# Performance work log

Hardware: AMD Instinct MI355X
Metric: run time of the kernel (lower is better)

## Reference

```python
import jax, jax.numpy as jnp
import numpy as np

B, D_IN, C, P = 8192, 2048, 1000, 256


def setup_inputs() -> dict:
    key = jax.random.key(0)
    ks = jax.random.split(key, 6)
    return {
        "x": jax.random.normal(ks[0], (B, D_IN), dtype=jnp.float32),
        "Wm": jax.random.normal(ks[1], (C, D_IN), dtype=jnp.float32) * (1.0 / np.sqrt(D_IN)),
        "bm": jax.random.normal(ks[2], (C,), dtype=jnp.float32) * 0.01,
        "u": jax.random.normal(ks[3], (P, C), dtype=jnp.float32),
        "v": jax.random.normal(ks[4], (P, C), dtype=jnp.float32),
        "w": jax.random.normal(ks[5], (P, 1), dtype=jnp.float32),
    }


def reference(x, Wm, bm, u, v, w):
    # Backbone: Linear(D_IN -> C) producing per-instance logits (B, C)
    preds = jnp.einsum("bd,cd->bc", x, Wm) + bm
    # Gated attention, fully batched (replaces per-instance Python loop):
    # tanh(u @ pred) * sigmoid(v @ pred)  -> (B, P)
    gated = jnp.tanh(jnp.einsum("bc,pc->bp", preds, u)) * jax.nn.sigmoid(
        jnp.einsum("bc,pc->bp", preds, v)
    )
    scores = (gated @ w).ravel()          # (B,)
    attention = jax.nn.softmax(scores)    # softmax over instances
    total_pred = jnp.sum(preds * attention[:, None])
    return preds, total_pred
```

## Files before the change

### kernel.cpp

```cpp
#include <hip/hip_runtime.h>
#include <hip/hip_fp16.h>

typedef _Float16 half8 __attribute__((ext_vector_type(8)));
typedef float f32x4 __attribute__((ext_vector_type(4)));

#define B_   8192
#define DIN  2048
#define C_   1000
#define CP   1024
#define NP2  512

static const size_t OFF_WH  = 0;
static const size_t OFF_UVH = OFF_WH  + (size_t)CP * DIN * 2;
static const size_t OFF_PH  = OFF_UVH + (size_t)NP2 * CP * 2;
static const size_t OFF_SC  = OFF_PH  + (size_t)B_ * CP * 2;
static const size_t OFF_RS  = OFF_SC  + (size_t)B_ * 4;
static const size_t WS_NEED = OFF_RS  + (size_t)B_ * 4;

__device__ __forceinline__ void gload16(const void* g, void* l) {
  __builtin_amdgcn_global_load_lds(
      (const __attribute__((address_space(1))) void*)g,
      (__attribute__((address_space(3))) void*)l, 16, 0, 0);
}

__global__ __launch_bounds__(256) void prep_kernel(
    const float* __restrict__ Wm,
    const float* __restrict__ u, const float* __restrict__ v,
    _Float16* __restrict__ wh, _Float16* __restrict__ uvh,
    float* __restrict__ scores, float* __restrict__ rowsum)
{
  const long NW  = (long)CP * DIN / 8;
  const long NUV = (long)NP2 * CP / 8;
  const long NZ  = 2 * (long)B_ / 8;
  const long T   = NW + NUV + NZ;
  for (long idx = (long)blockIdx.x * blockDim.x + threadIdx.x; idx < T;
       idx += (long)gridDim.x * blockDim.x) {
    if (idx < NW) {
      long e = idx * 8;
      int row = (int)(e >> 11);
      half8 h;
      if (row < C_) {
        float4 p0 = *(const float4*)(Wm + e);
        float4 p1 = *(const float4*)(Wm + e + 4);
        h[0] = (_Float16)p0.x; h[1] = (_Float16)p0.y; h[2] = (_Float16)p0.z; h[3] = (_Float16)p0.w;
        h[4] = (_Float16)p1.x; h[5] = (_Float16)p1.y; h[6] = (_Float16)p1.z; h[7] = (_Float16)p1.w;
      } else {
        h = (half8)(_Float16)0.f;
      }
      *(half8*)(wh + e) = h;
    } else if (idx < NW + NUV) {
      long e = (idx - NW) * 8;
      int j = (int)(e >> 10);
      int k = (int)(e & 1023);
      const float* src = (j & 1) ? v : u;
      int p = j >> 1;
      half8 h;
      #pragma unroll
      for (int t = 0; t < 8; ++t) {
        int kk = k + t;
        h[t] = (kk < C_) ? (_Float16)src[(size_t)p * C_ + kk] : (_Float16)0.f;
      }
      *(half8*)(uvh + e) = h;
    } else {
      long e = (idx - NW - NUV) * 8;
      float4 z = {0.f, 0.f, 0.f, 0.f};
      if (e < B_) {
        *(float4*)(scores + e) = z; *(float4*)(scores + e + 4) = z;
      } else {
        long r = e - B_;
        *(float4*)(rowsum + r) = z; *(float4*)(rowsum + r + 4) = z;
      }
    }
  }
}

__global__ __launch_bounds__(256) void gemm1_kernel(
    const float* __restrict__ x, const _Float16* __restrict__ wh,
    const float* __restrict__ bmv, float* __restrict__ preds,
    _Float16* __restrict__ predsh, float* __restrict__ rowsum)
{
  __shared__ _Float16 sA[2][128 * 64];
  __shared__ _Float16 sB[2][128 * 64];
  const int tid  = threadIdx.x;
  const int lane = tid & 63;
  const int w    = tid >> 6;
  const int wm   = w >> 1, wn = w & 1;
  const int bm0  = blockIdx.x * 128;
  const int bn0  = blockIdx.y * 128;

  f32x4 acc[4][4] = {};

  const float* srcA[4];
  int dstAoff[4];
  #pragma unroll
  for (int i = 0; i < 4; ++i) {
    int slot = i * 256 + tid;
    int row  = slot >> 3;
    int cb   = (slot & 7) << 4;
    dstAoff[i] = row * 128 + (cb ^ ((row & 7) << 4));
    srcA[i] = x + (size_t)(bm0 + row) * DIN + (slot & 7) * 8;
  }
  const _Float16* srcB[4];
  #pragma unroll
  for (int i = 0; i < 4; ++i) {
    int slot = i * 256 + tid;
    int row  = slot >> 3;
    int cb   = (slot & 7) << 4;
    int scb  = cb ^ ((row & 7) << 4);
    srcB[i] = wh + (size_t)(bn0 + row) * DIN + (scb >> 1);
  }
  int aoff[4][2], boff[4][2];
  #pragma unroll
  for (int mi = 0; mi < 4; ++mi) {
    #pragma unroll
    for (int ks = 0; ks < 2; ++ks) {
      int kb = ks * 64 + (lane >> 4) * 16;
      int ra = wm * 64 + mi * 16 + (lane & 15);
      aoff[mi][ks] = ra * 128 + (kb ^ ((ra & 7) << 4));
      int rb = wn * 64 + mi * 16 + (lane & 15);
      boff[mi][ks] = rb * 128 + (kb ^ ((rb & 7) << 4));
    }
  }

  float4 ra[4][2];
  auto loadA = [&]() {
    #pragma unroll
    for (int i = 0; i < 4; ++i) {
      ra[i][0] = *(const float4*)(srcA[i]);
      ra[i][1] = *(const float4*)(srcA[i] + 4);
      srcA[i] += 64;
    }
  };
  auto writeA = [&](int c) {
    #pragma unroll
    for (int i = 0; i < 4; ++i) {
      half8 h;
      h[0] = (_Float16)ra[i][0].x; h[1] = (_Float16)ra[i][0].y;
      h[2] = (_Float16)ra[i][0].z; h[3] = (_Float16)ra[i][0].w;
      h[4] = (_Float16)ra[i][1].x; h[5] = (_Float16)ra[i][1].y;
      h[6] = (_Float16)ra[i][1].z; h[7] = (_Float16)ra[i][1].w;
      *(half8*)((char*)&sA[c][0] + dstAoff[i]) = h;
    }
  };
  auto stageB = [&](int c) {
    #pragma unroll
    for (int i = 0; i < 4; ++i) {
      gload16(srcB[i], &sB[c][(i * 4 + w) * 512]);
      srcB[i] += 64;
    }
  };
  auto compute = [&](int c) {
    const char* bA = (const char*)&sA[c][0];
    const char* bB = (const char*)&sB[c][0];
    #pragma unroll
    for (int ks = 0; ks < 2; ++ks) {
      half8 a[4], b[4];
      #pragma unroll
      for (int mi = 0; mi < 4; ++mi) a[mi] = *(const half8*)(bA + aoff[mi][ks]);
      #pragma unroll
      for (int ni = 0; ni < 4; ++ni) b[ni] = *(const half8*)(bB + boff[ni][ks]);
      #pragma unroll
      for (int mi = 0; mi < 4; ++mi)
        #pragma unroll
        for (int ni = 0; ni < 4; ++ni)
          acc[mi][ni] = __builtin_amdgcn_mfma_f32_16x16x32_f16(a[mi], b[ni], acc[mi][ni], 0, 0, 0);
    }
  };

  const int NT = DIN / 64;

  loadA();
  stageB(0);
  writeA(0);
  asm volatile("s_waitcnt vmcnt(0) lgkmcnt(0)" ::: "memory");
  __builtin_amdgcn_s_barrier();

  #pragma unroll 1
  for (int t = 0; t < NT - 1; ++t) {
    const int c = t & 1;
    loadA();
    stageB(c ^ 1);
    asm volatile("s_waitcnt vmcnt(12)" ::: "memory");
    __builtin_amdgcn_s_barrier();
    compute(c);
    writeA(c ^ 1);
    asm volatile("s_waitcnt lgkmcnt(0)" ::: "memory");
    __builtin_amdgcn_s_barrier();
  }
  asm volatile("s_waitcnt vmcnt(0)" ::: "memory");
  __builtin_amdgcn_s_barrier();
  compute((NT - 1) & 1);

  float rp[4][4] = {};
  #pragma unroll
  for (int mi = 0; mi < 4; ++mi) {
    #pragma unroll
    for (int ni = 0; ni < 4; ++ni) {
      f32x4 d = acc[mi][ni];
      int gc = bn0 + wn * 64 + ni * 16 + (lane & 15);
      float bias = (gc < C_) ? bmv[gc] : 0.f;
      #pragma unroll
      for (int j = 0; j < 4; ++j) {
        int gr = bm0 + wm * 64 + mi * 16 + (lane >> 4) * 4 + j;
        float val = d[j] + bias;
        predsh[(size_t)gr * CP + gc] = (_Float16)val;
        if (gc < C_) preds[(size_t)gr * C_ + gc] = val;
        rp[mi][j] += val;
      }
    }
  }
  #pragma unroll
  for (int mi = 0; mi < 4; ++mi) {
    #pragma unroll
    for (int j = 0; j < 4; ++j) {
      float s = rp[mi][j];
      s += __shfl_xor(s, 1); s += __shfl_xor(s, 2);
      s += __shfl_xor(s, 4); s += __shfl_xor(s, 8);
      if ((lane & 15) == 0) {
        int gr = bm0 + wm * 64 + mi * 16 + (lane >> 4) * 4 + j;
        atomicAdd(&rowsum[gr], s);
      }
    }
  }
}

__global__ __launch_bounds__(256) void gemm2_kernel(
    const _Float16* __restrict__ predsh, const _Float16* __restrict__ uvh,
    const float* __restrict__ wv, float* __restrict__ scores)
{
  __shared__ _Float16 sA[2][64 * 64];
  __shared__ _Float16 sB[2][128 * 64];
  const int tid  = threadIdx.x;
  const int lane = tid & 63;
  const int w    = tid >> 6;
  const int wm   = w >> 1, wn = w & 1;
  const int bm0  = blockIdx.x * 64;
  const int bn0  = blockIdx.y * 128;

  f32x4 acc[2][4] = {};

  const _Float16* srcA[2]; const _Float16* srcB[4];
  #pragma unroll
  for (int i = 0; i < 2; ++i) {
    int slot = i * 256 + tid;
    int row  = slot >> 3;
    int cb   = (slot & 7) << 4;
    int scb  = cb ^ ((row & 7) << 4);
    srcA[i] = predsh + (size_t)(bm0 + row) * CP + (scb >> 1);
  }
  #pragma unroll
  for (int i = 0; i < 4; ++i) {
    int slot = i * 256 + tid;
    int row  = slot >> 3;
    int cb   = (slot & 7) << 4;
    int scb  = cb ^ ((row & 7) << 4);
    srcB[i] = uvh + (size_t)(bn0 + row) * CP + (scb >> 1);
  }
  int aoff[2][2], boff[4][2];
  #pragma unroll
  for (int ks = 0; ks < 2; ++ks) {
    int kb = ks * 64 + (lane >> 4) * 16;
    #pragma unroll
    for (int mi = 0; mi < 2; ++mi) {
      int ra = wm * 32 + mi * 16 + (lane & 15);
      aoff[mi][ks] = ra * 128 + (kb ^ ((ra & 7) << 4));
    }
    #pragma unroll
    for (int ni = 0; ni < 4; ++ni) {
      int rb = wn * 64 + ni * 16 + (lane & 15);
      boff[ni][ks] = rb * 128 + (kb ^ ((rb & 7) << 4));
    }
  }

  auto stage = [&](int c) {
    #pragma unroll
    for (int i = 0; i < 2; ++i) {
      gload16(srcA[i], &sA[c][(i * 4 + w) * 512]);
      srcA[i] += 64;
    }
    #pragma unroll
    for (int i = 0; i < 4; ++i) {
      gload16(srcB[i], &sB[c][(i * 4 + w) * 512]);
      srcB[i] += 64;
    }
  };

  auto compute = [&](int c) {
    const char* bA = (const char*)&sA[c][0];
    const char* bB = (const char*)&sB[c][0];
    #pragma unroll
    for (int ks = 0; ks < 2; ++ks) {
      half8 a[2], b[4];
      #pragma unroll
      for (int mi = 0; mi < 2; ++mi) a[mi] = *(const half8*)(bA + aoff[mi][ks]);
      #pragma unroll
      for (int ni = 0; ni < 4; ++ni) b[ni] = *(const half8*)(bB + boff[ni][ks]);
      #pragma unroll
      for (int mi = 0; mi < 2; ++mi)
        #pragma unroll
        for (int ni = 0; ni < 4; ++ni)
          acc[mi][ni] = __builtin_amdgcn_mfma_f32_16x16x32_f16(a[mi], b[ni], acc[mi][ni], 0, 0, 0);
    }
  };

  const int NT = CP / 64;
  stage(0);
  #pragma unroll 1
  for (int kt = 0; kt < NT; kt += 2) {
    stage(1);
    asm volatile("s_waitcnt vmcnt(6)" ::: "memory");
    __builtin_amdgcn_s_barrier();
    compute(0);
    __builtin_amdgcn_s_barrier();
    if (kt + 2 < NT) {
      stage(0);
      asm volatile("s_waitcnt vmcnt(6)" ::: "memory");
    } else {
      asm volatile("s_waitcnt vmcnt(0)" ::: "memory");
    }
    __builtin_amdgcn_s_barrier();
    compute(1);
    __builtin_amdgcn_s_barrier();
  }

  float sp[2][4] = {};
  #pragma unroll
  for (int mi = 0; mi < 2; ++mi) {
    #pragma unroll
    for (int ni = 0; ni < 4; ++ni) {
      f32x4 d = acc[mi][ni];
      int gc = bn0 + wn * 64 + ni * 16 + (lane & 15);
      float wq = wv[gc >> 1];
      bool even = ((gc & 1) == 0);
      #pragma unroll
      for (int j = 0; j < 4; ++j) {
        float t  = d[j];
        float pr = __shfl_xor(t, 1);
        float th = 2.f / (1.f + __expf(-2.f * t)) - 1.f;
        float sg = 1.f / (1.f + __expf(-pr));
        sp[mi][j] += even ? (th * sg * wq) : 0.f;
      }
    }
  }
  #pragma unroll
  for (int mi = 0; mi < 2; ++mi) {
    #pragma unroll
    for (int j = 0; j < 4; ++j) {
      float s = sp[mi][j];
      s += __shfl_xor(s, 1); s += __shfl_xor(s, 2);
      s += __shfl_xor(s, 4); s += __shfl_xor(s, 8);
      if ((lane & 15) == 0) {
        int gr = bm0 + wm * 32 + mi * 16 + (lane >> 4) * 4 + j;
        atomicAdd(&scores[gr], s);
      }
    }
  }
}

__global__ __launch_bounds__(1024) void final_kernel(
    const float* __restrict__ scores, const float* __restrict__ rowsum,
    float* __restrict__ out)
{
  __shared__ float red[16], red2[16];
  const int t = threadIdx.x;
  const int lane = t & 63, wid = t >> 6;
  float s[8];
  float m = -3.4e38f;
  #pragma unroll
  for (int i = 0; i < 8; ++i) { s[i] = scores[t + i * 1024]; m = fmaxf(m, s[i]); }
  #pragma unroll
  for (int off = 1; off < 64; off <<= 1) m = fmaxf(m, __shfl_xor(m, off));
  if (lane == 0) red[wid] = m;
  __syncthreads();
  #pragma unroll
  for (int i = 0; i < 16; ++i) m = fmaxf(m, red[i]);
  __syncthreads();

  float se = 0.f, sr = 0.f;
  #pragma unroll
  for (int i = 0; i < 8; ++i) {
    float e = __expf(s[i] - m);
    se += e;
    sr += e * rowsum[t + i * 1024];
  }
  #pragma unroll
  for (int off = 1; off < 64; off <<= 1) { se += __shfl_xor(se, off); sr += __shfl_xor(sr, off); }
  if (lane == 0) { red[wid] = se; red2[wid] = sr; }
  __syncthreads();
  if (t == 0) {
    float tse = 0.f, tsr = 0.f;
    for (int i = 0; i < 16; ++i) { tse += red[i]; tsr += red2[i]; }
    out[0] = tsr / tse;
  }
}

extern "C" void kernel_launch(void* const* d_in, const int* in_sizes, int n_in,
                              void* d_out, int out_size, void* d_ws, size_t ws_size,
                              hipStream_t stream)
{
  const float* x   = (const float*)d_in[0];
  const float* Wm  = (const float*)d_in[1];
  const float* bmv = (const float*)d_in[2];
  const float* u   = (const float*)d_in[3];
  const float* v   = (const float*)d_in[4];
  const float* wv  = (const float*)d_in[5];
  float* out = (float*)d_out;

  if (ws_size < WS_NEED) return;

  char* ws = (char*)d_ws;
  _Float16* wh     = (_Float16*)(ws + OFF_WH);
  _Float16* uvh    = (_Float16*)(ws + OFF_UVH);
  _Float16* predsh = (_Float16*)(ws + OFF_PH);
  float*    scores = (float*)(ws + OFF_SC);
  float*    rowsum = (float*)(ws + OFF_RS);

  prep_kernel<<<1288, 256, 0, stream>>>(Wm, u, v, wh, uvh, scores, rowsum);
  gemm1_kernel<<<dim3(64, 8), 256, 0, stream>>>(x, wh, bmv, out, predsh, rowsum);
  gemm2_kernel<<<dim3(128, 4), 256, 0, stream>>>(predsh, uvh, wv, scores);
  final_kernel<<<1, 1024, 0, stream>>>(scores, rowsum, out + (size_t)B_ * C_);
}
```

Measured before the change: 92.93 us.

## Restructure gemm1 into 512-thread triple-buffered pipeline with fp32 LDS staging

Rewrites the first GEMM so that fp32 x tiles are loaded straight into LDS with global_load_lds, and the fp16 conversion happens after LDS reads rather than through registers. Each block now has 512 threads covering 256 rows, k-steps are 32, and a three-deep buffer ring lets fragment reads for the next step overlap MFMAs on the current one. MFMA sections are wrapped in raised wave priority. The goal is to hide global load latency and drop the register round-trip for A, at the cost of more LDS (about 120KB) and twice as many LDS bytes read for A.

```diff
diff --git a/kernel.cpp b/kernel.cpp
--- a/kernel.cpp
+++ b/kernel.cpp
@@ -16,6 +16,12 @@
 static const size_t OFF_SC  = OFF_PH  + (size_t)B_ * CP * 2;
 static const size_t OFF_RS  = OFF_SC  + (size_t)B_ * 4;
 static const size_t WS_NEED = OFF_RS  + (size_t)B_ * 4;
+
+#define FENCE asm volatile("" ::: "memory")
+#define BARRIER do { FENCE; __builtin_amdgcn_s_barrier(); FENCE; } while (0)
+#define VMCNT(n) asm volatile("s_waitcnt vmcnt(" #n ")" ::: "memory")
+#define PRIO1 __builtin_amdgcn_s_setprio(1)
+#define PRIO0 __builtin_amdgcn_s_setprio(0)
 
 __device__ __forceinline__ void gload16(const void* g, void* l) {
   __builtin_amdgcn_global_load_lds(
@@ -74,150 +80,140 @@
   }
 }
 
-__global__ __launch_bounds__(256) void gemm1_kernel(
+__global__ __launch_bounds__(512, 2) void gemm1_kernel(
     const float* __restrict__ x, const _Float16* __restrict__ wh,
     const float* __restrict__ bmv, float* __restrict__ preds,
     _Float16* __restrict__ predsh, float* __restrict__ rowsum)
 {
-  __shared__ _Float16 sA[2][128 * 64];
-  __shared__ _Float16 sB[2][128 * 64];
+  __shared__ __align__(16) char LB[3 * 32768 + 3 * 8192];
   const int tid  = threadIdx.x;
   const int lane = tid & 63;
   const int w    = tid >> 6;
-  const int wm   = w >> 1, wn = w & 1;
-  const int bm0  = blockIdx.x * 128;
+  const int wm   = w >> 1;
+  const int wn   = w & 1;
+  const int bm0  = blockIdx.x * 256;
   const int bn0  = blockIdx.y * 128;
 
   f32x4 acc[4][4] = {};
 
-  const float* srcA[4];
-  int dstAoff[4];
-  #pragma unroll
-  for (int i = 0; i < 4; ++i) {
-    int slot = i * 256 + tid;
-    int row  = slot >> 3;
-    int cb   = (slot & 7) << 4;
-    dstAoff[i] = row * 128 + (cb ^ ((row & 7) << 4));
-    srcA[i] = x + (size_t)(bm0 + row) * DIN + (slot & 7) * 8;
-  }
-  const _Float16* srcB[4];
-  #pragma unroll
-  for (int i = 0; i < 4; ++i) {
-    int slot = i * 256 + tid;
-    int row  = slot >> 3;
-    int cb   = (slot & 7) << 4;
-    int scb  = cb ^ ((row & 7) << 4);
-    srcB[i] = wh + (size_t)(bn0 + row) * DIN + (scb >> 1);
-  }
-  int aoff[4][2], boff[4][2];
-  #pragma unroll
-  for (int mi = 0; mi < 4; ++mi) {
-    #pragma unroll
-    for (int ks = 0; ks < 2; ++ks) {
-      int kb = ks * 64 + (lane >> 4) * 16;
-      int ra = wm * 64 + mi * 16 + (lane & 15);
-      aoff[mi][ks] = ra * 128 + (kb ^ ((ra & 7) << 4));
-      int rb = wn * 64 + mi * 16 + (lane & 15);
-      boff[mi][ks] = rb * 128 + (kb ^ ((rb & 7) << 4));
-    }
-  }
-
-  float4 ra[4][2];
-  auto loadA = [&]() {
-    #pragma unroll
-    for (int i = 0; i < 4; ++i) {
-      ra[i][0] = *(const float4*)(srcA[i]);
-      ra[i][1] = *(const float4*)(srcA[i] + 4);
-      srcA[i] += 64;
-    }
+  const int trow = tid >> 3;
+  const float* pAx = x + (size_t)(bm0 + trow) * DIN + (((tid & 7) ^ (trow & 7)) << 2);
+  const int brow = tid >> 2;
+  const _Float16* pBx = wh + (size_t)(bn0 + brow) * DIN + ((((tid & 3) ^ ((brow >> 1) & 3)) << 3));
+
+  int aoff[4][2], boff[4];
+  #pragma unroll
+  for (int m = 0; m < 4; ++m) {
+    int ra = wm * 64 + m * 16 + (lane & 15);
+    int c0 = (lane >> 4) * 2;
+    aoff[m][0] = ra * 128 + (((c0)     ^ (ra & 7)) << 4);
+    aoff[m][1] = ra * 128 + (((c0 + 1) ^ (ra & 7)) << 4);
+  }
+  #pragma unroll
+  for (int n = 0; n < 4; ++n) {
+    int rb = wn * 64 + n * 16 + (lane & 15);
+    boff[n] = rb * 64 + ((((lane >> 4)) ^ ((rb >> 1) & 3)) << 4);
+  }
+
+  half8 Aa[4], Ba[4], Ab[4], Bb[4];
+
+  auto stage = [&](int c) {
+    #pragma unroll
+    for (int k = 0; k < 4; ++k)
+      gload16(pAx + (size_t)k * 64 * DIN, LB + c * 32768 + k * 8192 + w * 1024);
+    gload16(pBx, LB + 98304 + c * 8192 + w * 1024);
+    pAx += 32; pBx += 32;
   };
-  auto writeA = [&](int c) {
-    #pragma unroll
-    for (int i = 0; i < 4; ++i) {
+  auto rdFrag = [&](int c, half8 (&A)[4], half8 (&Bf)[4]) {
+    const char* ab = LB + c * 32768;
+    const char* bb = LB + 98304 + c * 8192;
+    #pragma unroll
+    for (int m = 0; m < 4; ++m) {
+      f32x4 lo = *(const f32x4*)(ab + aoff[m][0]);
+      f32x4 hi = *(const f32x4*)(ab + aoff[m][1]);
       half8 h;
-      h[0] = (_Float16)ra[i][0].x; h[1] = (_Float16)ra[i][0].y;
-      h[2] = (_Float16)ra[i][0].z; h[3] = (_Float16)ra[i][0].w;
-      h[4] = (_Float16)ra[i][1].x; h[5] = (_Float16)ra[i][1].y;
-      h[6] = (_Float16)ra[i][1].z; h[7] = (_Float16)ra[i][1].w;
-      *(half8*)((char*)&sA[c][0] + dstAoff[i]) = h;
-    }
+      h[0] = (_Float16)lo[0]; h[1] = (_Float16)lo[1];
+      h[2] = (_Float16)lo[2]; h[3] = (_Float16)lo[3];
+      h[4] = (_Float16)hi[0]; h[5] = (_Float16)hi[1];
+      h[6] = (_Float16)hi[2]; h[7] = (_Float16)hi[3];
+      A[m] = h;
+    }
+    #pragma unroll
+    for (int n = 0; n < 4; ++n)
+      Bf[n] = *(const half8*)(bb + boff[n]);
   };
-  auto stageB = [&](int c) {
-    #pragma unroll
-    for (int i = 0; i < 4; ++i) {
-      gload16(srcB[i], &sB[c][(i * 4 + w) * 512]);
-      srcB[i] += 64;
-    }
+  auto mfAll = [&](half8 (&A)[4], half8 (&Bf)[4]) {
+    PRIO1;
+    #pragma unroll
+    for (int m = 0; m < 4; ++m)
+      #pragma unroll
+      for (int n = 0; n < 4; ++n)
+        acc[m][n] = __builtin_amdgcn_mfma_f32_16x16x32_f16(A[m], Bf[n], acc[m][n], 0, 0, 0);
+    PRIO0;
   };
-  auto compute = [&](int c) {
-    const char* bA = (const char*)&sA[c][0];
-    const char* bB = (const char*)&sB[c][0];
-    #pragma unroll
-    for (int ks = 0; ks < 2; ++ks) {
-      half8 a[4], b[4];
-      #pragma unroll
-      for (int mi = 0; mi < 4; ++mi) a[mi] = *(const half8*)(bA + aoff[mi][ks]);
-      #pragma unroll
-      for (int ni = 0; ni < 4; ++ni) b[ni] = *(const half8*)(bB + boff[ni][ks]);
-      #pragma unroll
-      for (int mi = 0; mi < 4; ++mi)
-        #pragma unroll
-        for (int ni = 0; ni < 4; ++ni)
-          acc[mi][ni] = __builtin_amdgcn_mfma_f32_16x16x32_f16(a[mi], b[ni], acc[mi][ni], 0, 0, 0);
-    }
-  };
-
-  const int NT = DIN / 64;
-
-  loadA();
-  stageB(0);
-  writeA(0);
-  asm volatile("s_waitcnt vmcnt(0) lgkmcnt(0)" ::: "memory");
-  __builtin_amdgcn_s_barrier();
-
+
+  stage(0);
+  stage(1);
+  VMCNT(5);
+  BARRIER;
+  rdFrag(0, Aa, Ba);
+
+  int c0 = 0;
   #pragma unroll 1
-  for (int t = 0; t < NT - 1; ++t) {
-    const int c = t & 1;
-    loadA();
-    stageB(c ^ 1);
-    asm volatile("s_waitcnt vmcnt(12)" ::: "memory");
-    __builtin_amdgcn_s_barrier();
-    compute(c);
-    writeA(c ^ 1);
-    asm volatile("s_waitcnt lgkmcnt(0)" ::: "memory");
-    __builtin_amdgcn_s_barrier();
-  }
-  asm volatile("s_waitcnt vmcnt(0)" ::: "memory");
-  __builtin_amdgcn_s_barrier();
-  compute((NT - 1) & 1);
+  for (int t = 0; t < 62; t += 2) {
+    const int c1 = (c0 == 2) ? 0 : c0 + 1;
+    const int c2 = (c1 == 2) ? 0 : c1 + 1;
+
+    stage(c2);
+    VMCNT(5);
+    BARRIER;
+    rdFrag(c1, Ab, Bb);
+    mfAll(Aa, Ba);
+    BARRIER;
+
+    stage(c0);
+    VMCNT(5);
+    BARRIER;
+    rdFrag(c2, Aa, Ba);
+    mfAll(Ab, Bb);
+    BARRIER;
+
+    c0 = c2;
+  }
+
+  VMCNT(0);
+  BARRIER;
+  rdFrag(0, Ab, Bb);
+  mfAll(Aa, Ba);
+  mfAll(Ab, Bb);
 
   float rp[4][4] = {};
   #pragma unroll
-  for (int mi = 0; mi < 4; ++mi) {
-    #pragma unroll
-    for (int ni = 0; ni < 4; ++ni) {
-      f32x4 d = acc[mi][ni];
-      int gc = bn0 + wn * 64 + ni * 16 + (lane & 15);
+  for (int m = 0; m < 4; ++m) {
+    #pragma unroll
+    for (int n = 0; n < 4; ++n) {
+      f32x4 d = acc[m][n];
+      int gc = bn0 + wn * 64 + n * 16 + (lane & 15);
       float bias = (gc < C_) ? bmv[gc] : 0.f;
       #pragma unroll
       for (int j = 0; j < 4; ++j) {
-        int gr = bm0 + wm * 64 + mi * 16 + (lane >> 4) * 4 + j;
+        int gr = bm0 + wm * 64 + m * 16 + (lane >> 4) * 4 + j;
         float val = d[j] + bias;
         predsh[(size_t)gr * CP + gc] = (_Float16)val;
         if (gc < C_) preds[(size_t)gr * C_ + gc] = val;
-        rp[mi][j] += val;
-      }
-    }
-  }
-  #pragma unroll
-  for (int mi = 0; mi < 4; ++mi) {
+        rp[m][j] += val;
+      }
+    }
+  }
+  #pragma unroll
+  for (int m = 0; m < 4; ++m) {
     #pragma unroll
     for (int j = 0; j < 4; ++j) {
-      float s = rp[mi][j];
+      float s = rp[m][j];
       s += __shfl_xor(s, 1); s += __shfl_xor(s, 2);
       s += __shfl_xor(s, 4); s += __shfl_xor(s, 8);
       if ((lane & 15) == 0) {
-        int gr = bm0 + wm * 64 + mi * 16 + (lane >> 4) * 4 + j;
+        int gr = bm0 + wm * 64 + m * 16 + (lane >> 4) * 4 + j;
         atomicAdd(&rowsum[gr], s);
       }
     }
@@ -309,18 +305,18 @@
   for (int kt = 0; kt < NT; kt += 2) {
     stage(1);
     asm volatile("s_waitcnt vmcnt(6)" ::: "memory");
-    __builtin_amdgcn_s_barrier();
+    BARRIER;
     compute(0);
-    __builtin_amdgcn_s_barrier();
+    BARRIER;
     if (kt + 2 < NT) {
       stage(0);
       asm volatile("s_waitcnt vmcnt(6)" ::: "memory");
     } else {
       asm volatile("s_waitcnt vmcnt(0)" ::: "memory");
     }
-    __builtin_amdgcn_s_barrier();
+    BARRIER;
     compute(1);
-    __builtin_amdgcn_s_barrier();
+    BARRIER;
   }
 
   float sp[2][4] = {};
@@ -416,7 +412,7 @@
   float*    rowsum = (float*)(ws + OFF_RS);
 
   prep_kernel<<<1288, 256, 0, stream>>>(Wm, u, v, wh, uvh, scores, rowsum);
-  gemm1_kernel<<<dim3(64, 8), 256, 0, stream>>>(x, wh, bmv, out, predsh, rowsum);
+  gemm1_kernel<<<dim3(32, 8), 512, 0, stream>>>(x, wh, bmv, out, predsh, rowsum);
   gemm2_kernel<<<dim3(128, 4), 256, 0, stream>>>(predsh, uvh, wv, scores);
   final_kernel<<<1, 1024, 0, stream>>>(scores, rowsum, out + (size_t)B_ * C_);
 }
```

New measurement: 93.59 us. Within noise of the previous version (+0.7%).
